# Kernel tuning notes

Hardware: AMD Instinct MI355X
Metric: run time of the kernel (lower is better)

Reference implementation:

```python
import jax, jax.numpy as jnp
import numpy as np

K_DIM = 768
HEADS = 8
HEAD_DIM = K_DIM // HEADS  # 96


def setup_inputs() -> dict:
    key = jax.random.key(0)
    ks = jax.random.split(key, 6)
    b, t = 4, 2048
    scale = 1.0 / np.sqrt(HEAD_DIM)
    return {
        "input_x": jax.random.normal(ks[0], (b, t, K_DIM), dtype=jnp.float32),
        "Wq": jax.random.normal(ks[1], (HEAD_DIM, HEAD_DIM), dtype=jnp.float32) * scale,
        "Wk": jax.random.normal(ks[2], (HEAD_DIM, HEAD_DIM), dtype=jnp.float32) * scale,
        "Wv": jax.random.normal(ks[3], (HEAD_DIM, HEAD_DIM), dtype=jnp.float32) * scale,
        "Wu": jax.random.normal(ks[4], (K_DIM, K_DIM), dtype=jnp.float32) * (1.0 / np.sqrt(K_DIM)),
        "bu": jax.random.normal(ks[5], (K_DIM,), dtype=jnp.float32) * 0.01,
    }


def reference(input_x, Wq, Wk, Wv, Wu, bu):
    b, t, k = input_x.shape
    h, d = HEADS, k // HEADS
    # split into heads: [b, t, h, d]; per-head projections share the same d x d weights
    x = input_x.reshape(b, t, h, d)
    inv4 = 1.0 / (k ** 0.25)
    q = jnp.einsum("bthd,od->btho", x, Wq) * inv4  # scaled queries
    kk = jnp.einsum("bthd,od->btho", x, Wk) * inv4  # scaled keys
    v = jnp.einsum("bthd,od->btho", x, Wv)
    # full attention matrix [b, h, t, t] (materialized, as in the original bmm impl)
    scores = jnp.einsum("bthd,bshd->bhts", q, kk)
    attn = jax.nn.softmax(scores, axis=-1)
    out = jnp.einsum("bhts,bshd->bthd", attn, v).reshape(b, t, k)
    return out @ Wu.T + bu
```

## Files before the change

kernel.cpp:

```cpp
#include <hip/hip_runtime.h>
#include <hip/hip_bf16.h>
#include <math.h>

#define TB 2048
#define NB 4
#define NH 8
#define HD 96
#define KD 768

typedef unsigned short u16;
typedef __attribute__((ext_vector_type(4))) u16 u16x4;
typedef __attribute__((ext_vector_type(8))) u16 u16x8;
typedef __attribute__((ext_vector_type(4))) float f32x4;
typedef __attribute__((ext_vector_type(16))) float f32x16;
typedef __attribute__((ext_vector_type(4))) unsigned u32x4;
typedef __attribute__((ext_vector_type(8))) __bf16 bf16x8;

__device__ __forceinline__ u16 f2bf(float f) {
    unsigned u = __builtin_bit_cast(unsigned, f);
    u += 0x7FFFu + ((u >> 16) & 1u);
    return (u16)(u >> 16);
}
__device__ __forceinline__ bf16x8 cast8(u16x8 u) { return __builtin_bit_cast(bf16x8, u); }
__device__ __forceinline__ unsigned pkbf(float a, float b) {
    unsigned w;
    asm("v_cvt_pk_bf16_f32 %0, %1, %2" : "=v"(w) : "v"(a), "v"(b));
    return w;
}

__global__ __launch_bounds__(256) void qkv_proj(
    const float* __restrict__ x, const float* __restrict__ Wq,
    const float* __restrict__ Wk, const float* __restrict__ Wv,
    u16* __restrict__ Q, u16* __restrict__ Kout, u16* __restrict__ VT, float inv4)
{
    __shared__ __align__(16) u16 Wl[3][96][104];
    const int tid = threadIdx.x;
    for (int idx = tid; idx < 3 * 9216; idx += 256) {
        int m = idx / 9216, rem = idx % 9216;
        const float* Wsrc = (m == 0) ? Wq : (m == 1) ? Wk : Wv;
        float scale = (m < 2) ? inv4 : 1.0f;
        int r = rem / 96, c = rem % 96;
        Wl[m][r][c] = f2bf(Wsrc[rem] * scale);
    }
    __syncthreads();

    const int w = tid >> 6, l = tid & 63;
    const int lc = l & 15, lk = l >> 4;
    const int bh = blockIdx.y, b = bh >> 3, h = bh & 7;
    const int t0 = blockIdx.x * 64 + w * 16;

    bf16x8 afrag[3];
    {
        const float* xp = x + ((long)((b * TB + t0 + lc) * NH + h)) * HD + 8 * lk;
#pragma unroll
        for (int c = 0; c < 3; ++c) {
            f32x4 f0 = *(const f32x4*)(xp + c * 32);
            f32x4 f1 = *(const f32x4*)(xp + c * 32 + 4);
            u16x8 u;
#pragma unroll
            for (int j = 0; j < 4; ++j) { u[j] = f2bf(f0[j]); u[4 + j] = f2bf(f1[j]); }
            afrag[c] = cast8(u);
        }
    }

    const f32x4 Z4 = {0.f, 0.f, 0.f, 0.f};
    u16* outs[2] = {Q, Kout};
#pragma unroll
    for (int m = 0; m < 2; ++m) {
        f32x4 acc[6];
#pragma unroll
        for (int nt = 0; nt < 6; ++nt) acc[nt] = Z4;
#pragma unroll
        for (int c = 0; c < 3; ++c) {
#pragma unroll
            for (int nt = 0; nt < 6; ++nt) {
                u16x8 bw = *(const u16x8*)&Wl[m][nt * 16 + lc][c * 32 + 8 * lk];
                acc[nt] = __builtin_amdgcn_mfma_f32_16x16x32_bf16(afrag[c], cast8(bw), acc[nt], 0, 0, 0);
            }
        }
#pragma unroll
        for (int reg = 0; reg < 4; ++reg) {
            int t = t0 + lk * 4 + reg;
            u16* op = outs[m] + ((long)bh * TB + t) * HD;
#pragma unroll
            for (int nt = 0; nt < 6; ++nt)
                op[nt * 16 + lc] = f2bf(acc[nt][reg]);
        }
    }
    {
        f32x4 acc[6];
#pragma unroll
        for (int nt = 0; nt < 6; ++nt) acc[nt] = Z4;
#pragma unroll
        for (int c = 0; c < 3; ++c) {
#pragma unroll
            for (int nt = 0; nt < 6; ++nt) {
                u16x8 aw = *(const u16x8*)&Wl[2][nt * 16 + lc][c * 32 + 8 * lk];
                acc[nt] = __builtin_amdgcn_mfma_f32_16x16x32_bf16(cast8(aw), afrag[c], acc[nt], 0, 0, 0);
            }
        }
#pragma unroll
        for (int nt = 0; nt < 6; ++nt)
#pragma unroll
            for (int reg = 0; reg < 4; ++reg) {
                int o = nt * 16 + lk * 4 + reg;
                VT[((long)bh * HD + o) * TB + t0 + lc] = f2bf(acc[nt][reg]);
            }
    }
}

__global__ __launch_bounds__(512) void attn(
    const u16* __restrict__ Q, const u16* __restrict__ Kin, const u16* __restrict__ VT,
    u16* __restrict__ O)
{
    __shared__ __align__(16) u16 Kl[64][104];
    __shared__ __align__(16) u16 Vt[96][72];

    const int tid = threadIdx.x;
    const int w = tid >> 6, l = tid & 63;
    const int m32 = l & 31, hi = l >> 5;
    const int bh = blockIdx.y;
    const int q0 = blockIdx.x * 256 + w * 32;

    const u16* Qb = Q + (long)bh * TB * HD;
    const u16* Kb = Kin + (long)bh * TB * HD;
    const u16* Vb = VT + (long)bh * HD * TB;

    const u16* gbase[3]; u16* lptr[3]; int mult[3];
#pragma unroll
    for (int ci = 0; ci < 3; ++ci) {
        int ch = tid + ci * 512;
        if (ch < 768) {
            int row = ch / 12, cc = (ch % 12) * 8;
            gbase[ci] = Kb + row * HD + cc;
            mult[ci] = HD;
            lptr[ci] = &Kl[row][cc];
        } else {
            int c2 = ch - 768;
            int d = c2 >> 3, sc = (c2 & 7) * 8;
            gbase[ci] = Vb + (long)d * TB + sc;
            mult[ci] = 1;
            lptr[ci] = &Vt[d][sc];
        }
    }

    bf16x8 qb[6];
#pragma unroll
    for (int kk = 0; kk < 6; ++kk)
        qb[kk] = cast8(*(const u16x8*)(Qb + (long)(q0 + m32) * HD + kk * 16 + 8 * hi));

    u16x8 r[3];
#pragma unroll
    for (int ci = 0; ci < 3; ++ci) r[ci] = *(const u16x8*)(gbase[ci]);

    float m_st = -1e30f, l_st = 0.f;
    f32x16 accO[3];
#pragma unroll
    for (int dt = 0; dt < 3; ++dt)
#pragma unroll
        for (int rr = 0; rr < 16; ++rr) accO[dt][rr] = 0.f;

    for (int st = 0; st < TB / 64; ++st) {
        __syncthreads();
#pragma unroll
        for (int ci = 0; ci < 3; ++ci) *(u16x8*)lptr[ci] = r[ci];
        int s1 = (st + 1) * 64; if (s1 > TB - 64) s1 = TB - 64;
#pragma unroll
        for (int ci = 0; ci < 3; ++ci) r[ci] = *(const u16x8*)(gbase[ci] + (long)s1 * mult[ci]);
        __syncthreads();

        f32x16 sa[2];
#pragma unroll
        for (int st2 = 0; st2 < 2; ++st2) {
#pragma unroll
            for (int rr = 0; rr < 16; ++rr) sa[st2][rr] = 0.f;
#pragma unroll
            for (int kk = 0; kk < 6; ++kk) {
                u16x8 kf = *(const u16x8*)&Kl[st2 * 32 + m32][kk * 16 + 8 * hi];
                sa[st2] = __builtin_amdgcn_mfma_f32_32x32x16_bf16(cast8(kf), qb[kk], sa[st2], 0, 0, 0);
            }
        }

        float tm = sa[0][0];
#pragma unroll
        for (int st2 = 0; st2 < 2; ++st2)
#pragma unroll
            for (int rr = 0; rr < 16; ++rr) tm = fmaxf(tm, sa[st2][rr]);
        tm = fmaxf(tm, __shfl_xor(tm, 32));
        if (!__all(tm - m_st <= 8.0f)) {
            float mnew = fmaxf(m_st, tm);
            float alpha = __expf(m_st - mnew);
#pragma unroll
            for (int dt = 0; dt < 3; ++dt)
#pragma unroll
                for (int rr = 0; rr < 16; ++rr) accO[dt][rr] *= alpha;
            l_st *= alpha;
            m_st = mnew;
        }
        float sum = 0.f;
#pragma unroll
        for (int st2 = 0; st2 < 2; ++st2)
#pragma unroll
            for (int rr = 0; rr < 16; ++rr) {
                float pv = __expf(sa[st2][rr] - m_st);
                sa[st2][rr] = pv;
                sum += pv;
            }
        sum += __shfl_xor(sum, 32);
        l_st += sum;

#pragma unroll
        for (int st2 = 0; st2 < 2; ++st2) {
            unsigned A1 = pkbf(sa[st2][0], sa[st2][1]);
            unsigned A2 = pkbf(sa[st2][2], sa[st2][3]);
            unsigned B1 = pkbf(sa[st2][4], sa[st2][5]);
            unsigned B2 = pkbf(sa[st2][6], sa[st2][7]);
            unsigned A3 = pkbf(sa[st2][8], sa[st2][9]);
            unsigned A4 = pkbf(sa[st2][10], sa[st2][11]);
            unsigned B3 = pkbf(sa[st2][12], sa[st2][13]);
            unsigned B4 = pkbf(sa[st2][14], sa[st2][15]);
            unsigned xA1 = __shfl_xor((int)A1, 32), xA2 = __shfl_xor((int)A2, 32);
            unsigned xB1 = __shfl_xor((int)B1, 32), xB2 = __shfl_xor((int)B2, 32);
            unsigned xA3 = __shfl_xor((int)A3, 32), xA4 = __shfl_xor((int)A4, 32);
            unsigned xB3 = __shfl_xor((int)B3, 32), xB4 = __shfl_xor((int)B4, 32);
            u32x4 t0 = { hi ? xB1 : A1, hi ? xB2 : A2, hi ? B1 : xA1, hi ? B2 : xA2 };
            u32x4 t1 = { hi ? xB3 : A3, hi ? xB4 : A4, hi ? B3 : xA3, hi ? B4 : xA4 };
            bf16x8 pb0 = __builtin_bit_cast(bf16x8, t0);
            bf16x8 pb1 = __builtin_bit_cast(bf16x8, t1);
#pragma unroll
            for (int dt = 0; dt < 3; ++dt) {
                u16x8 vfa = *(const u16x8*)&Vt[dt * 32 + m32][st2 * 32 + 8 * hi];
                accO[dt] = __builtin_amdgcn_mfma_f32_32x32x16_bf16(cast8(vfa), pb0, accO[dt], 0, 0, 0);
            }
#pragma unroll
            for (int dt = 0; dt < 3; ++dt) {
                u16x8 vfb = *(const u16x8*)&Vt[dt * 32 + m32][st2 * 32 + 16 + 8 * hi];
                accO[dt] = __builtin_amdgcn_mfma_f32_32x32x16_bf16(cast8(vfb), pb1, accO[dt], 0, 0, 0);
            }
        }
    }

    const int b = bh >> 3, h = bh & 7;
    float linv = 1.0f / l_st;
    int t = q0 + m32;
    u16* op = O + ((long)(b * TB + t)) * KD + h * HD;
#pragma unroll
    for (int dt = 0; dt < 3; ++dt)
#pragma unroll
        for (int q4 = 0; q4 < 4; ++q4) {
            u16x4 v = { f2bf(accO[dt][q4 * 4 + 0] * linv), f2bf(accO[dt][q4 * 4 + 1] * linv),
                        f2bf(accO[dt][q4 * 4 + 2] * linv), f2bf(accO[dt][q4 * 4 + 3] * linv) };
            *(u16x4*)(op + dt * 32 + q4 * 8 + 4 * hi) = v;
        }
}

__global__ __launch_bounds__(256) void wu_conv(const float* __restrict__ Wu, u16* __restrict__ Wub) {
    int i = (blockIdx.x * 256 + threadIdx.x) * 4;
    f32x4 f = *(const f32x4*)(Wu + i);
    u16x4 o = { f2bf(f[0]), f2bf(f[1]), f2bf(f[2]), f2bf(f[3]) };
    *(u16x4*)(Wub + i) = o;
}

__global__ __launch_bounds__(256) void out_gemm(
    const u16* __restrict__ O, const u16* __restrict__ Wub,
    const float* __restrict__ bu, float* __restrict__ out)
{
    __shared__ __align__(16) u16 Al[64][40];
    __shared__ __align__(16) u16 Bl[128][40];
    const int tid = threadIdx.x;
    const int w = tid >> 6, l = tid & 63;
    const int lc = l & 15, lk = l >> 4;
    const int m0 = blockIdx.x * 64, n0 = blockIdx.y * 128;

    const int arow = tid >> 2, acc_ = (tid & 3) * 8;
    const int brow0 = tid >> 2, bcc0 = (tid & 3) * 8;
    const int brow1 = (tid + 256) >> 2, bcc1 = (tid & 3) * 8;

    f32x4 acc[8];
    const f32x4 Z4 = {0.f, 0.f, 0.f, 0.f};
#pragma unroll
    for (int nt = 0; nt < 8; ++nt) acc[nt] = Z4;

    u16x8 ra = *(const u16x8*)(O + (long)(m0 + arow) * KD + acc_);
    u16x8 rb0 = *(const u16x8*)(Wub + (long)(n0 + brow0) * KD + bcc0);
    u16x8 rb1 = *(const u16x8*)(Wub + (long)(n0 + brow1) * KD + bcc1);

    for (int c0 = 0; c0 < KD; c0 += 32) {
        __syncthreads();
        *(u16x8*)&Al[arow][acc_] = ra;
        *(u16x8*)&Bl[brow0][bcc0] = rb0;
        *(u16x8*)&Bl[brow1][bcc1] = rb1;
        int cn = c0 + 32; if (cn > KD - 32) cn = KD - 32;
        ra = *(const u16x8*)(O + (long)(m0 + arow) * KD + cn + acc_);
        rb0 = *(const u16x8*)(Wub + (long)(n0 + brow0) * KD + cn + bcc0);
        rb1 = *(const u16x8*)(Wub + (long)(n0 + brow1) * KD + cn + bcc1);
        __syncthreads();

        bf16x8 a = cast8(*(const u16x8*)&Al[w * 16 + lc][8 * lk]);
#pragma unroll
        for (int nt = 0; nt < 8; ++nt) {
            u16x8 bb = *(const u16x8*)&Bl[nt * 16 + lc][8 * lk];
            acc[nt] = __builtin_amdgcn_mfma_f32_16x16x32_bf16(a, cast8(bb), acc[nt], 0, 0, 0);
        }
    }

#pragma unroll
    for (int reg = 0; reg < 4; ++reg) {
        int rr = m0 + w * 16 + lk * 4 + reg;
        float* op = out + (long)rr * KD + n0;
#pragma unroll
        for (int nt = 0; nt < 8; ++nt)
            op[nt * 16 + lc] = acc[nt][reg] + bu[n0 + nt * 16 + lc];
    }
}

extern "C" void kernel_launch(void* const* d_in, const int* in_sizes, int n_in,
                              void* d_out, int out_size, void* d_ws, size_t ws_size,
                              hipStream_t stream) {
    const float* x  = (const float*)d_in[0];
    const float* Wq = (const float*)d_in[1];
    const float* Wk = (const float*)d_in[2];
    const float* Wv = (const float*)d_in[3];
    const float* Wu = (const float*)d_in[4];
    const float* bu = (const float*)d_in[5];
    float* out = (float*)d_out;

    u16* ws = (u16*)d_ws;
    const size_t SZ = (size_t)NB * NH * TB * HD;
    u16* Q   = ws;
    u16* Kq  = ws + SZ;
    u16* VT  = ws + 2 * SZ;
    u16* O   = ws + 3 * SZ;
    u16* Wub = ws;

    const float inv4 = 1.0f / powf((float)KD, 0.25f);

    qkv_proj<<<dim3(TB / 64, NB * NH), dim3(256), 0, stream>>>(x, Wq, Wk, Wv, Q, Kq, VT, inv4);
    attn<<<dim3(TB / 256, NB * NH), dim3(512), 0, stream>>>(Q, Kq, VT, O);
    wu_conv<<<dim3((KD * KD) / 1024), dim3(256), 0, stream>>>(Wu, Wub);
    out_gemm<<<dim3((NB * TB) / 64, KD / 128), dim3(256), 0, stream>>>(O, Wub, bu, out);
}
```

Measured before the change: 199.3 us.

## Double-buffer attention and output GEMM LDS tiles, retile GEMM, remap blocks

The attention kernel now uses 256-thread blocks over 128 queries and double-buffers its K/V tiles in shared memory, so each step needs one barrier instead of two. Block indices are remapped to interleave work across XCDs, and s_setprio is raised around the MFMA sections. The output GEMM is rewritten as 128x128 tiles with 32x32x16 MFMAs, a k-step of 64, double-buffered LDS and the same XCD-aware block remapping. This increases LDS use per block, which may lower occupancy, in exchange for more reuse per load and fewer synchronizations.

```diff
diff --git a/kernel.cpp b/kernel.cpp
--- a/kernel.cpp
+++ b/kernel.cpp
@@ -109,38 +109,42 @@
     }
 }
 
-__global__ __launch_bounds__(512) void attn(
+#define KOFF 0
+#define VOFF (64 * 104)
+#define SLAB (64 * 104 + 96 * 72)
+
+__global__ __launch_bounds__(256) void attn(
     const u16* __restrict__ Q, const u16* __restrict__ Kin, const u16* __restrict__ VT,
     u16* __restrict__ O)
 {
-    __shared__ __align__(16) u16 Kl[64][104];
-    __shared__ __align__(16) u16 Vt[96][72];
+    __shared__ __align__(16) u16 SM[2][SLAB];
 
     const int tid = threadIdx.x;
     const int w = tid >> 6, l = tid & 63;
     const int m32 = l & 31, hi = l >> 5;
-    const int bh = blockIdx.y;
-    const int q0 = blockIdx.x * 256 + w * 32;
+    const int lid = (blockIdx.x & 7) * 64 + (blockIdx.x >> 3);
+    const int qt = lid & 15, bh = lid >> 4;
+    const int q0 = qt * 128 + w * 32;
 
     const u16* Qb = Q + (long)bh * TB * HD;
     const u16* Kb = Kin + (long)bh * TB * HD;
     const u16* Vb = VT + (long)bh * HD * TB;
 
-    const u16* gbase[3]; u16* lptr[3]; int mult[3];
-#pragma unroll
-    for (int ci = 0; ci < 3; ++ci) {
-        int ch = tid + ci * 512;
+    const u16* gbase[6]; int loff[6]; int mult[6];
+#pragma unroll
+    for (int ci = 0; ci < 6; ++ci) {
+        int ch = tid + ci * 256;
         if (ch < 768) {
             int row = ch / 12, cc = (ch % 12) * 8;
             gbase[ci] = Kb + row * HD + cc;
             mult[ci] = HD;
-            lptr[ci] = &Kl[row][cc];
+            loff[ci] = KOFF + row * 104 + cc;
         } else {
             int c2 = ch - 768;
             int d = c2 >> 3, sc = (c2 & 7) * 8;
             gbase[ci] = Vb + (long)d * TB + sc;
             mult[ci] = 1;
-            lptr[ci] = &Vt[d][sc];
+            loff[ci] = VOFF + d * 72 + sc;
         }
     }
 
@@ -149,9 +153,13 @@
     for (int kk = 0; kk < 6; ++kk)
         qb[kk] = cast8(*(const u16x8*)(Qb + (long)(q0 + m32) * HD + kk * 16 + 8 * hi));
 
-    u16x8 r[3];
-#pragma unroll
-    for (int ci = 0; ci < 3; ++ci) r[ci] = *(const u16x8*)(gbase[ci]);
+    u16x8 r[6];
+#pragma unroll
+    for (int ci = 0; ci < 6; ++ci) r[ci] = *(const u16x8*)(gbase[ci]);
+#pragma unroll
+    for (int ci = 0; ci < 6; ++ci) *(u16x8*)(SM[0] + loff[ci]) = r[ci];
+#pragma unroll
+    for (int ci = 0; ci < 6; ++ci) r[ci] = *(const u16x8*)(gbase[ci] + (long)64 * mult[ci]);
 
     float m_st = -1e30f, l_st = 0.f;
     f32x16 accO[3];
@@ -162,24 +170,30 @@
 
     for (int st = 0; st < TB / 64; ++st) {
         __syncthreads();
-#pragma unroll
-        for (int ci = 0; ci < 3; ++ci) *(u16x8*)lptr[ci] = r[ci];
-        int s1 = (st + 1) * 64; if (s1 > TB - 64) s1 = TB - 64;
-#pragma unroll
-        for (int ci = 0; ci < 3; ++ci) r[ci] = *(const u16x8*)(gbase[ci] + (long)s1 * mult[ci]);
-        __syncthreads();
+        if (st < TB / 64 - 1) {
+            u16* dst = SM[(st + 1) & 1];
+#pragma unroll
+            for (int ci = 0; ci < 6; ++ci) *(u16x8*)(dst + loff[ci]) = r[ci];
+            int s2 = (st + 2 < TB / 64 ? st + 2 : TB / 64 - 1) * 64;
+#pragma unroll
+            for (int ci = 0; ci < 6; ++ci) r[ci] = *(const u16x8*)(gbase[ci] + (long)s2 * mult[ci]);
+        }
+        const u16* KP = SM[st & 1] + KOFF;
+        const u16* VP = SM[st & 1] + VOFF;
 
         f32x16 sa[2];
+        __builtin_amdgcn_s_setprio(1);
 #pragma unroll
         for (int st2 = 0; st2 < 2; ++st2) {
 #pragma unroll
             for (int rr = 0; rr < 16; ++rr) sa[st2][rr] = 0.f;
 #pragma unroll
             for (int kk = 0; kk < 6; ++kk) {
-                u16x8 kf = *(const u16x8*)&Kl[st2 * 32 + m32][kk * 16 + 8 * hi];
+                u16x8 kf = *(const u16x8*)(KP + (st2 * 32 + m32) * 104 + kk * 16 + 8 * hi);
                 sa[st2] = __builtin_amdgcn_mfma_f32_32x32x16_bf16(cast8(kf), qb[kk], sa[st2], 0, 0, 0);
             }
         }
+        __builtin_amdgcn_s_setprio(0);
 
         float tm = sa[0][0];
 #pragma unroll
@@ -227,16 +241,18 @@
             u32x4 t1 = { hi ? xB3 : A3, hi ? xB4 : A4, hi ? B3 : xA3, hi ? B4 : xA4 };
             bf16x8 pb0 = __builtin_bit_cast(bf16x8, t0);
             bf16x8 pb1 = __builtin_bit_cast(bf16x8, t1);
+            __builtin_amdgcn_s_setprio(1);
 #pragma unroll
             for (int dt = 0; dt < 3; ++dt) {
-                u16x8 vfa = *(const u16x8*)&Vt[dt * 32 + m32][st2 * 32 + 8 * hi];
+                u16x8 vfa = *(const u16x8*)(VP + (dt * 32 + m32) * 72 + st2 * 32 + 8 * hi);
                 accO[dt] = __builtin_amdgcn_mfma_f32_32x32x16_bf16(cast8(vfa), pb0, accO[dt], 0, 0, 0);
             }
 #pragma unroll
             for (int dt = 0; dt < 3; ++dt) {
-                u16x8 vfb = *(const u16x8*)&Vt[dt * 32 + m32][st2 * 32 + 16 + 8 * hi];
+                u16x8 vfb = *(const u16x8*)(VP + (dt * 32 + m32) * 72 + st2 * 32 + 16 + 8 * hi);
                 accO[dt] = __builtin_amdgcn_mfma_f32_32x32x16_bf16(cast8(vfb), pb1, accO[dt], 0, 0, 0);
             }
+            __builtin_amdgcn_s_setprio(0);
         }
     }
 
@@ -265,53 +281,93 @@
     const u16* __restrict__ O, const u16* __restrict__ Wub,
     const float* __restrict__ bu, float* __restrict__ out)
 {
-    __shared__ __align__(16) u16 Al[64][40];
-    __shared__ __align__(16) u16 Bl[128][40];
+    __shared__ __align__(16) u16 Al[2][128][68];
+    __shared__ __align__(16) u16 Bl[2][128][68];
     const int tid = threadIdx.x;
     const int w = tid >> 6, l = tid & 63;
-    const int lc = l & 15, lk = l >> 4;
-    const int m0 = blockIdx.x * 64, n0 = blockIdx.y * 128;
-
-    const int arow = tid >> 2, acc_ = (tid & 3) * 8;
-    const int brow0 = tid >> 2, bcc0 = (tid & 3) * 8;
-    const int brow1 = (tid + 256) >> 2, bcc1 = (tid & 3) * 8;
-
-    f32x4 acc[8];
-    const f32x4 Z4 = {0.f, 0.f, 0.f, 0.f};
-#pragma unroll
-    for (int nt = 0; nt < 8; ++nt) acc[nt] = Z4;
-
-    u16x8 ra = *(const u16x8*)(O + (long)(m0 + arow) * KD + acc_);
-    u16x8 rb0 = *(const u16x8*)(Wub + (long)(n0 + brow0) * KD + bcc0);
-    u16x8 rb1 = *(const u16x8*)(Wub + (long)(n0 + brow1) * KD + bcc1);
-
-    for (int c0 = 0; c0 < KD; c0 += 32) {
+    const int m32 = l & 31, hi = l >> 5;
+    const int wr = w >> 1, wc = w & 1;
+    const int lid = (blockIdx.x & 7) * 48 + (blockIdx.x >> 3);
+    const int nb = lid % 6, mb = lid / 6;
+    const int m0 = mb * 128, n0 = nb * 128;
+
+    const int crow = tid >> 3, ccol = (tid & 7) * 8;
+
+    f32x16 acc[2][2];
+#pragma unroll
+    for (int i = 0; i < 2; ++i)
+#pragma unroll
+        for (int j = 0; j < 2; ++j)
+#pragma unroll
+            for (int rr = 0; rr < 16; ++rr) acc[i][j][rr] = 0.f;
+
+    u16x8 ra[4], rb[4];
+#pragma unroll
+    for (int i = 0; i < 4; ++i) {
+        ra[i] = *(const u16x8*)(O   + (long)(m0 + crow + i * 32) * KD + ccol);
+        rb[i] = *(const u16x8*)(Wub + (long)(n0 + crow + i * 32) * KD + ccol);
+    }
+#pragma unroll
+    for (int i = 0; i < 4; ++i) {
+        *(u16x8*)&Al[0][crow + i * 32][ccol] = ra[i];
+        *(u16x8*)&Bl[0][crow + i * 32][ccol] = rb[i];
+    }
+#pragma unroll
+    for (int i = 0; i < 4; ++i) {
+        ra[i] = *(const u16x8*)(O   + (long)(m0 + crow + i * 32) * KD + 64 + ccol);
+        rb[i] = *(const u16x8*)(Wub + (long)(n0 + crow + i * 32) * KD + 64 + ccol);
+    }
+
+    for (int kt = 0; kt < KD / 64; ++kt) {
         __syncthreads();
-        *(u16x8*)&Al[arow][acc_] = ra;
-        *(u16x8*)&Bl[brow0][bcc0] = rb0;
-        *(u16x8*)&Bl[brow1][bcc1] = rb1;
-        int cn = c0 + 32; if (cn > KD - 32) cn = KD - 32;
-        ra = *(const u16x8*)(O + (long)(m0 + arow) * KD + cn + acc_);
-        rb0 = *(const u16x8*)(Wub + (long)(n0 + brow0) * KD + cn + bcc0);
-        rb1 = *(const u16x8*)(Wub + (long)(n0 + brow1) * KD + cn + bcc1);
-        __syncthreads();
-
-        bf16x8 a = cast8(*(const u16x8*)&Al[w * 16 + lc][8 * lk]);
-#pragma unroll
-        for (int nt = 0; nt < 8; ++nt) {
-            u16x8 bb = *(const u16x8*)&Bl[nt * 16 + lc][8 * lk];
-            acc[nt] = __builtin_amdgcn_mfma_f32_16x16x32_bf16(a, cast8(bb), acc[nt], 0, 0, 0);
-        }
-    }
-
-#pragma unroll
-    for (int reg = 0; reg < 4; ++reg) {
-        int rr = m0 + w * 16 + lk * 4 + reg;
-        float* op = out + (long)rr * KD + n0;
-#pragma unroll
-        for (int nt = 0; nt < 8; ++nt)
-            op[nt * 16 + lc] = acc[nt][reg] + bu[n0 + nt * 16 + lc];
-    }
+        if (kt < KD / 64 - 1) {
+            int p = (kt + 1) & 1;
+#pragma unroll
+            for (int i = 0; i < 4; ++i) {
+                *(u16x8*)&Al[p][crow + i * 32][ccol] = ra[i];
+                *(u16x8*)&Bl[p][crow + i * 32][ccol] = rb[i];
+            }
+            int cn = (kt + 2 < KD / 64 ? kt + 2 : KD / 64 - 1) * 64;
+#pragma unroll
+            for (int i = 0; i < 4; ++i) {
+                ra[i] = *(const u16x8*)(O   + (long)(m0 + crow + i * 32) * KD + cn + ccol);
+                rb[i] = *(const u16x8*)(Wub + (long)(n0 + crow + i * 32) * KD + cn + ccol);
+            }
+        }
+        int p = kt & 1;
+        __builtin_amdgcn_s_setprio(1);
+#pragma unroll
+        for (int k16 = 0; k16 < 4; ++k16) {
+            bf16x8 afr[2], bfr[2];
+#pragma unroll
+            for (int rb2 = 0; rb2 < 2; ++rb2)
+                afr[rb2] = cast8(*(const u16x8*)&Al[p][wr * 64 + rb2 * 32 + m32][k16 * 16 + 8 * hi]);
+#pragma unroll
+            for (int cb2 = 0; cb2 < 2; ++cb2)
+                bfr[cb2] = cast8(*(const u16x8*)&Bl[p][wc * 64 + cb2 * 32 + m32][k16 * 16 + 8 * hi]);
+#pragma unroll
+            for (int rb2 = 0; rb2 < 2; ++rb2)
+#pragma unroll
+                for (int cb2 = 0; cb2 < 2; ++cb2)
+                    acc[rb2][cb2] = __builtin_amdgcn_mfma_f32_32x32x16_bf16(afr[rb2], bfr[cb2], acc[rb2][cb2], 0, 0, 0);
+        }
+        __builtin_amdgcn_s_setprio(0);
+    }
+
+    const float bv0 = bu[n0 + wc * 64 + m32];
+    const float bv1 = bu[n0 + wc * 64 + 32 + m32];
+#pragma unroll
+    for (int rb2 = 0; rb2 < 2; ++rb2)
+#pragma unroll
+        for (int cb2 = 0; cb2 < 2; ++cb2) {
+            float bv = cb2 ? bv1 : bv0;
+            int nn = n0 + wc * 64 + cb2 * 32 + m32;
+#pragma unroll
+            for (int reg = 0; reg < 16; ++reg) {
+                int mm = m0 + wr * 64 + rb2 * 32 + (reg & 3) + 8 * (reg >> 2) + 4 * hi;
+                out[(long)mm * KD + nn] = acc[rb2][cb2][reg] + bv;
+            }
+        }
 }
 
 extern "C" void kernel_launch(void* const* d_in, const int* in_sizes, int n_in,
@@ -336,7 +392,7 @@
     const float inv4 = 1.0f / powf((float)KD, 0.25f);
 
     qkv_proj<<<dim3(TB / 64, NB * NH), dim3(256), 0, stream>>>(x, Wq, Wk, Wv, Q, Kq, VT, inv4);
-    attn<<<dim3(TB / 256, NB * NH), dim3(512), 0, stream>>>(Q, Kq, VT, O);
+    attn<<<dim3(TB / 128 * NB * NH), dim3(256), 0, stream>>>(Q, Kq, VT, O);
     wu_conv<<<dim3((KD * KD) / 1024), dim3(256), 0, stream>>>(Wu, Wub);
-    out_gemm<<<dim3((NB * TB) / 64, KD / 128), dim3(256), 0, stream>>>(O, Wub, bu, out);
-}
+    out_gemm<<<dim3((NB * TB / 128) * (KD / 128)), dim3(256), 0, stream>>>(O, Wub, bu, out);
+}
```

Result: slower. 208.8 us (+4.7%).
